# Performance work log

Measured on AMD Instinct MI355X. Metric: run time of the kernel, lower is better.

The kernel has to match this reference:

```python
import jax, jax.numpy as jnp
import numpy as np

TAU = 2.0        # LIF membrane time constant
VTH = 1.0        # spike threshold
VRESET = 0.0     # hard reset voltage
ALPHA = 2.0      # ATan surrogate alpha
LN_EPS = 1e-5


@jax.custom_vjp
def atan_spike(x):
    # Heaviside forward, ATan surrogate backward (spikingjelly surrogate.ATan)
    return (x >= 0.0).astype(x.dtype)

def _atan_fwd(x):
    return atan_spike(x), x

def _atan_bwd(x, g):
    z = (jnp.pi / 2.0) * ALPHA * x
    return (g * (ALPHA / 2.0) / (1.0 + z * z),)

atan_spike.defvjp(_atan_fwd, _atan_bwd)


def layer_norm(x, w, b):
    mu = jnp.mean(x, axis=-1, keepdims=True)
    var = jnp.mean(jnp.square(x - mu), axis=-1, keepdims=True)
    return (x - mu) * jax.lax.rsqrt(var + LN_EPS) * w + b


def time_shift(x):
    # x: [B,T,C] -> x shifted by one step in time, zero-padded at t=0
    return jnp.pad(x, ((0, 0), (1, 0), (0, 0)))[:, :-1]


def wkv(time_decay, time_first, k, v):
    # Numerically-stable RWKV WKV recurrence. k, v: [B,T,C]
    w = -jnp.exp(time_decay)  # [C]
    u = time_first            # [C]
    B, T, C = k.shape
    kT = jnp.moveaxis(k, 1, 0)  # [T,B,C]
    vT = jnp.moveaxis(v, 1, 0)
    init = (jnp.zeros((B, C), k.dtype),
            jnp.zeros((B, C), k.dtype),
            jnp.full((B, C), -1e38, k.dtype))

    def step(carry, kv_t):
        aa, bb, pp = carry
        kt, vt = kv_t
        ww = u + kt
        p = jnp.maximum(pp, ww)
        e1 = jnp.exp(pp - p)
        e2 = jnp.exp(ww - p)
        y = (e1 * aa + e2 * vt) / (e1 * bb + e2)
        ww2 = pp + w
        p2 = jnp.maximum(ww2, kt)
        e1b = jnp.exp(ww2 - p2)
        e2b = jnp.exp(kt - p2)
        return (e1b * aa + e2b * vt, e1b * bb + e2b, p2), y

    _, yT = jax.lax.scan(step, init, (kT, vT))
    return jnp.moveaxis(yT, 0, 1)  # [B,T,C]


def lif(x):
    # MultiStepLIFNode: tau=2, decay_input=True, v_th=1, hard reset to 0.
    # Recurrence runs over the sequence dim (permute(1,0,2) in torch is layout only).
    xT = jnp.moveaxis(x, 1, 0)  # [T,B,C]
    v0 = jnp.zeros_like(xT[0])

    def step(v, xt):
        v = v + (xt - (v - VRESET)) / TAU
        s = atan_spike(v - VTH)
        v = (1.0 - s) * v + s * VRESET
        return v, s

    _, sT = jax.lax.scan(step, v0, xT)
    return jnp.moveaxis(sT, 0, 1)


def rwkv_time_mix(x, time_decay, time_first, mix_k, mix_v, mix_r, Wk, Wv, Wr, Wo):
    xx = time_shift(x)
    xk = x * mix_k + xx * (1.0 - mix_k)
    xv = x * mix_v + xx * (1.0 - mix_v)
    xr = x * mix_r + xx * (1.0 - mix_r)
    k = jnp.einsum('btc,cd->btd', xk, Wk)
    v = jnp.einsum('btc,cd->btd', xv, Wv)
    r = jax.nn.sigmoid(jnp.einsum('btc,cd->btd', xr, Wr))
    y = wkv(time_decay, time_first, k, v)
    return jnp.einsum('btc,cd->btd', r * y, Wo)


def rwkv_channel_mix(x, mix_k, mix_r, Wk, Wv, Wr):
    xx = time_shift(x)
    xk = x * mix_k + xx * (1.0 - mix_k)
    xr = x * mix_r + xx * (1.0 - mix_r)
    k = jnp.square(jax.nn.relu(jnp.einsum('btc,ch->bth', xk, Wk)))  # relu^2
    kv = jnp.einsum('bth,hc->btc', k, Wv)
    return jax.nn.sigmoid(jnp.einsum('btc,cd->btd', xr, Wr)) * kv


def setup_inputs() -> dict:
    key = jax.random.key(0)
    B, T, C, H = 8, 2048, 768, 3072
    ks = jax.random.split(key, 20)
    p = lambda k, shape, s=0.02: (jax.random.normal(k, shape, jnp.float32) * s)
    u = lambda k, shape: jax.random.uniform(k, shape, jnp.float32)
    return {
        'x': jax.random.normal(ks[0], (B, T, C), jnp.float32),
        'ln1_w': jnp.ones((C,), jnp.float32), 'ln1_b': jnp.zeros((C,), jnp.float32),
        'ln2_w': jnp.ones((C,), jnp.float32), 'ln2_b': jnp.zeros((C,), jnp.float32),
        'att_time_decay': p(ks[1], (C,), 1.0),
        'att_time_first': p(ks[2], (C,), 1.0),
        'att_mix_k': u(ks[3], (C,)), 'att_mix_v': u(ks[4], (C,)), 'att_mix_r': u(ks[5], (C,)),
        'att_Wk': p(ks[6], (C, C)), 'att_Wv': p(ks[7], (C, C)),
        'att_Wr': p(ks[8], (C, C)), 'att_Wo': p(ks[9], (C, C)),
        'ffn_mix_k': u(ks[10], (C,)), 'ffn_mix_r': u(ks[11], (C,)),
        'ffn_Wk': p(ks[12], (C, H)), 'ffn_Wv': p(ks[13], (H, C)), 'ffn_Wr': p(ks[14], (C, C)),
    }


def reference(x, ln1_w, ln1_b, ln2_w, ln2_b,
              att_time_decay, att_time_first, att_mix_k, att_mix_v, att_mix_r,
              att_Wk, att_Wv, att_Wr, att_Wo,
              ffn_mix_k, ffn_mix_r, ffn_Wk, ffn_Wv, ffn_Wr):
    # Block.forward with layer_id != 0 (no ln0, att path); dropout in eval mode.
    a = rwkv_time_mix(layer_norm(x, ln1_w, ln1_b), att_time_decay, att_time_first,
                      att_mix_k, att_mix_v, att_mix_r, att_Wk, att_Wv, att_Wr, att_Wo)
    x = x + lif(a)
    f = rwkv_channel_mix(layer_norm(x, ln2_w, ln2_b), ffn_mix_k, ffn_mix_r,
                         ffn_Wk, ffn_Wv, ffn_Wr)
    x = x + lif(f)
    return x
```

## Files before the change

kernel.cpp:

```cpp
#include <hip/hip_runtime.h>

#define B_ 8
#define T_ 2048
#define C_ 768
#define H_ 3072
#define BT_ (B_ * T_)
#define BC_ (B_ * C_)
#define WSEG 64
#define NWSEG 32
#define LSEG 64
#define NLSEG 32
#define LWARM 96

typedef unsigned short u16;
typedef short bf16x8 __attribute__((ext_vector_type(8)));
typedef float f32x4 __attribute__((ext_vector_type(4)));

__device__ __forceinline__ float b2f(u16 u) {
    union { unsigned i; float f; } w; w.i = ((unsigned)u) << 16; return w.f;
}
__device__ __forceinline__ u16 f2b(float f) {
    union { float f; unsigned i; } w; w.f = f;
    return (u16)((w.i + 0x7fffu + ((w.i >> 16) & 1u)) >> 16);
}

typedef __attribute__((address_space(3))) unsigned int lds_u32;
typedef const __attribute__((address_space(1))) unsigned int glb_u32;
__device__ __forceinline__ void gld_lds16(const void* g, void* l) {
    __builtin_amdgcn_global_load_lds((glb_u32*)g, (lds_u32*)l, 16, 0, 0);
}

template<int NOUT>
__global__ __launch_bounds__(512)
void lnmixw(const float* __restrict__ x, const float* __restrict__ w,
            const float* __restrict__ b,
            const float* __restrict__ m1, const float* __restrict__ m2,
            const float* __restrict__ m3,
            u16* __restrict__ o1, u16* __restrict__ o2, u16* __restrict__ o3) {
    const int wv = threadIdx.x >> 6, lane = threadIdx.x & 63;
    const int row = blockIdx.x * 8 + wv;
    const int t = row % T_;
    const float4* xr4 = (const float4*)(x + (size_t)row * C_);
    const float4* xp4 = (const float4*)(x + (size_t)(row - 1) * C_);
    float4 c[3], p[3];
#pragma unroll
    for (int j = 0; j < 3; ++j) c[j] = xr4[lane + j * 64];
    if (t > 0) {
#pragma unroll
        for (int j = 0; j < 3; ++j) p[j] = xp4[lane + j * 64];
    } else {
#pragma unroll
        for (int j = 0; j < 3; ++j) p[j] = make_float4(0.f, 0.f, 0.f, 0.f);
    }
    float s = 0.f, s2 = 0.f, ps = 0.f, ps2 = 0.f;
#pragma unroll
    for (int j = 0; j < 3; ++j) {
        s += c[j].x + c[j].y + c[j].z + c[j].w;
        s2 += c[j].x * c[j].x + c[j].y * c[j].y + c[j].z * c[j].z + c[j].w * c[j].w;
        ps += p[j].x + p[j].y + p[j].z + p[j].w;
        ps2 += p[j].x * p[j].x + p[j].y * p[j].y + p[j].z * p[j].z + p[j].w * p[j].w;
    }
#pragma unroll
    for (int off = 32; off > 0; off >>= 1) {
        s += __shfl_down(s, off);  s2 += __shfl_down(s2, off);
        ps += __shfl_down(ps, off); ps2 += __shfl_down(ps2, off);
    }
    s = __shfl(s, 0); s2 = __shfl(s2, 0); ps = __shfl(ps, 0); ps2 = __shfl(ps2, 0);
    const float mu = s * (1.f / C_);
    const float rs = rsqrtf(s2 * (1.f / C_) - mu * mu + 1e-5f);
    const float pmu = ps * (1.f / C_);
    const float prs = rsqrtf(ps2 * (1.f / C_) - pmu * pmu + 1e-5f);
    const size_t ob = (size_t)row * C_;
#pragma unroll
    for (int j = 0; j < 3; ++j) {
        int fi = lane + j * 64;
        float4 w4 = ((const float4*)w)[fi];
        float4 b4 = ((const float4*)b)[fi];
        float4 n, np;
        n.x = (c[j].x - mu) * rs * w4.x + b4.x;
        n.y = (c[j].y - mu) * rs * w4.y + b4.y;
        n.z = (c[j].z - mu) * rs * w4.z + b4.z;
        n.w = (c[j].w - mu) * rs * w4.w + b4.w;
        if (t > 0) {
            np.x = (p[j].x - pmu) * prs * w4.x + b4.x;
            np.y = (p[j].y - pmu) * prs * w4.y + b4.y;
            np.z = (p[j].z - pmu) * prs * w4.z + b4.z;
            np.w = (p[j].w - pmu) * prs * w4.w + b4.w;
        } else {
            np = make_float4(0.f, 0.f, 0.f, 0.f);
        }
        float4 mm = ((const float4*)m1)[fi];
        ushort4 ov;
        ov.x = f2b(fmaf(mm.x, n.x - np.x, np.x));
        ov.y = f2b(fmaf(mm.y, n.y - np.y, np.y));
        ov.z = f2b(fmaf(mm.z, n.z - np.z, np.z));
        ov.w = f2b(fmaf(mm.w, n.w - np.w, np.w));
        *(ushort4*)(o1 + ob + fi * 4) = ov;
        mm = ((const float4*)m2)[fi];
        ov.x = f2b(fmaf(mm.x, n.x - np.x, np.x));
        ov.y = f2b(fmaf(mm.y, n.y - np.y, np.y));
        ov.z = f2b(fmaf(mm.z, n.z - np.z, np.z));
        ov.w = f2b(fmaf(mm.w, n.w - np.w, np.w));
        *(ushort4*)(o2 + ob + fi * 4) = ov;
        if constexpr (NOUT == 3) {
            mm = ((const float4*)m3)[fi];
            ov.x = f2b(fmaf(mm.x, n.x - np.x, np.x));
            ov.y = f2b(fmaf(mm.y, n.y - np.y, np.y));
            ov.z = f2b(fmaf(mm.z, n.z - np.z, np.z));
            ov.w = f2b(fmaf(mm.w, n.w - np.w, np.w));
            *(ushort4*)(o3 + ob + fi * 4) = ov;
        }
    }
}

struct TCJ { const float* s; u16* d; int R, Ncol, nbx, b0; };
struct TC7 { TCJ j[7]; };
__global__ void tcast_all(TC7 jobs) {
    __shared__ float t[32][33];
    int bid = blockIdx.x;
    int ji = 0;
#pragma unroll
    for (int k = 1; k < 7; ++k) if (bid >= jobs.j[k].b0) ji = k;
    TCJ jb = jobs.j[ji];
    int local = bid - jb.b0;
    int bx = local % jb.nbx, by = local / jb.nbx;
    int c0 = bx * 32, r0 = by * 32;
    int col = threadIdx.x & 31, rw = threadIdx.x >> 5;
#pragma unroll
    for (int i = 0; i < 4; ++i) {
        int r = rw + i * 8;
        t[r][col] = jb.s[(size_t)(r0 + r) * jb.Ncol + c0 + col];
    }
    __syncthreads();
#pragma unroll
    for (int i = 0; i < 4; ++i) {
        int r = rw + i * 8;
        jb.d[(size_t)(c0 + r) * jb.R + r0 + col] = f2b(t[col][r]);
    }
}

__device__ __forceinline__ void gemm_core128(const u16* __restrict__ A,
                                             const u16* __restrict__ WT,
                                             int K, int m0, int n0,
                                             u16* L, f32x4 acc[4][4]) {
    const int tid = threadIdx.x;
    const int lane = tid & 63, wid = tid >> 6;
    const int wr = wid >> 1, wc = wid & 1;
    const int r16 = lane & 15, g = lane >> 4;

    const int srow = tid >> 3;
    const int sunit = tid & 7;
    const int ssw = sunit ^ (srow & 7);
    const u16* gA = A + (size_t)(m0 + srow) * K + ssw * 8;
    const u16* gB = WT + (size_t)(n0 + srow) * K + ssw * 8;
    u16* lA = L + tid * 8;
    u16* lB = L + 8192 + tid * 8;

#define STGA(buf) do { \
        gld_lds16(gA,                  lA + (buf) * 16384); \
        gld_lds16(gA + (size_t)32 * K, lA + (buf) * 16384 + 2048); \
        gld_lds16(gA + (size_t)64 * K, lA + (buf) * 16384 + 4096); \
        gld_lds16(gA + (size_t)96 * K, lA + (buf) * 16384 + 6144); \
        gA += 64; } while (0)
#define STGB(buf) do { \
        gld_lds16(gB,                  lB + (buf) * 16384); \
        gld_lds16(gB + (size_t)32 * K, lB + (buf) * 16384 + 2048); \
        gld_lds16(gB + (size_t)64 * K, lB + (buf) * 16384 + 4096); \
        gld_lds16(gB + (size_t)96 * K, lB + (buf) * 16384 + 6144); \
        gB += 64; } while (0)

    int offA[4], offB[4];
#pragma unroll
    for (int m = 0; m < 4; ++m) {
        int row = wr * 64 + m * 16 + r16;
        offA[m] = row * 64 + (g ^ (row & 7)) * 8;
    }
#pragma unroll
    for (int n = 0; n < 4; ++n) {
        int rob = wc * 64 + n * 16 + r16;
        offB[n] = 8192 + rob * 64 + (g ^ (rob & 7)) * 8;
    }

    const int nt = K >> 6;
    STGA(0); STGB(0);
    asm volatile("s_waitcnt vmcnt(0)" ::: "memory");
    __builtin_amdgcn_sched_barrier(0);
    __builtin_amdgcn_s_barrier();

    for (int t = 0; t < nt; ++t) {
        const u16* Lb = L + (t & 1) * 16384;
        const bool stg = (t + 1 < nt);
        bf16x8 a0[4], b0[4];
#pragma unroll
        for (int m = 0; m < 4; ++m) a0[m] = *(const bf16x8*)(Lb + offA[m]);
#pragma unroll
        for (int n = 0; n < 4; ++n) b0[n] = *(const bf16x8*)(Lb + offB[n]);
        __builtin_amdgcn_sched_barrier(0);
        if (stg) { STGA((t + 1) & 1); STGB((t + 1) & 1); }
        asm volatile("s_waitcnt lgkmcnt(0)" ::: "memory");
        __builtin_amdgcn_sched_barrier(0);
        __builtin_amdgcn_s_setprio(1);
#pragma unroll
        for (int m = 0; m < 4; ++m)
#pragma unroll
            for (int n = 0; n < 4; ++n)
                acc[m][n] = __builtin_amdgcn_mfma_f32_16x16x32_bf16(a0[m], b0[n], acc[m][n], 0, 0, 0);
        __builtin_amdgcn_s_setprio(0);
        __builtin_amdgcn_sched_barrier(0);
        bf16x8 a1[4], b1[4];
#pragma unroll
        for (int m = 0; m < 4; ++m) a1[m] = *(const bf16x8*)(Lb + (offA[m] ^ 32));
#pragma unroll
        for (int n = 0; n < 4; ++n) b1[n] = *(const bf16x8*)(Lb + (offB[n] ^ 32));
        asm volatile("s_waitcnt lgkmcnt(0)" ::: "memory");
        __builtin_amdgcn_sched_barrier(0);
        __builtin_amdgcn_s_setprio(1);
#pragma unroll
        for (int m = 0; m < 4; ++m)
#pragma unroll
            for (int n = 0; n < 4; ++n)
                acc[m][n] = __builtin_amdgcn_mfma_f32_16x16x32_bf16(a1[m], b1[n], acc[m][n], 0, 0, 0);
        __builtin_amdgcn_s_setprio(0);
        __builtin_amdgcn_sched_barrier(0);
        if (stg) {
            asm volatile("s_waitcnt vmcnt(0)" ::: "memory");
            __builtin_amdgcn_sched_barrier(0);
            __builtin_amdgcn_s_barrier();
        }
    }
#undef STGA
#undef STGB
}

__device__ __forceinline__ void xcd_remap2(int& bx, int& by) {
    const int gx = gridDim.x;
    const int nwg = gx * gridDim.y;
    const int lin = blockIdx.y * gx + blockIdx.x;
    const int q = nwg >> 3, r = nwg & 7;
    const int xcd = lin & 7, pos = lin >> 3;
    const int nid = (xcd < r ? xcd * (q + 1) : r * (q + 1) + (xcd - r) * q) + pos;
    const int g4 = gx << 2;
    const int grp = nid / g4, rem = nid - grp * g4;
    by = (grp << 2) + (rem & 3);
    bx = rem >> 2;
}

__device__ __forceinline__ void epilogue128(f32x4 acc[4][4], u16* O, const u16* Emul,
                                            int m0, int n0, int N, int mode, bool emul) {
    const int lane = threadIdx.x & 63, wid = threadIdx.x >> 6;
    const int wr = wid >> 1, wc = wid & 1;
    const int r16 = lane & 15, g = lane >> 4;
#pragma unroll
    for (int m = 0; m < 4; ++m)
#pragma unroll
        for (int n = 0; n < 4; ++n)
#pragma unroll
            for (int j = 0; j < 4; ++j) {
                int row = m0 + wr * 64 + m * 16 + g * 4 + j;
                int col = n0 + wc * 64 + n * 16 + r16;
                float v = acc[m][n][j];
                if (mode == 1) v = 1.f / (1.f + expf(-v));
                else if (mode == 2) { v = fmaxf(v, 0.f); v = v * v; }
                size_t o = (size_t)row * N + col;
                if (emul) v *= b2f(Emul[o]);
                O[o] = f2b(v);
            }
}

template<int MODE, bool EMUL>
__global__ __launch_bounds__(256, 2)
void gemm128(const u16* __restrict__ A, const u16* __restrict__ WT,
             u16* __restrict__ Cout, const u16* __restrict__ Emul, int N, int K) {
    __shared__ u16 L[32768];
    int bx, by;
    xcd_remap2(bx, by);
    const int m0 = by << 7, n0 = bx << 7;
    f32x4 acc[4][4];
#pragma unroll
    for (int i = 0; i < 4; ++i)
#pragma unroll
        for (int j = 0; j < 4; ++j)
#pragma unroll
            for (int q = 0; q < 4; ++q) acc[i][j][q] = 0.f;
    gemm_core128(A, WT, K, m0, n0, L, acc);
    epilogue128(acc, Cout, Emul, m0, n0, N, MODE, EMUL);
}

struct P3 {
    const u16 *A0, *A1, *A2;
    const u16 *W0, *W1, *W2;
    u16 *O0, *O1, *O2;
};
__global__ __launch_bounds__(256, 2)
void proj3(P3 p, int N, int K) {
    __shared__ u16 L[32768];
    const int z = blockIdx.z;
    const u16* A = (z == 0) ? p.A0 : (z == 1) ? p.A1 : p.A2;
    const u16* W = (z == 0) ? p.W0 : (z == 1) ? p.W1 : p.W2;
    u16* O = (z == 0) ? p.O0 : (z == 1) ? p.O1 : p.O2;
    int bx, by;
    xcd_remap2(bx, by);
    const int m0 = by << 7, n0 = bx << 7;
    f32x4 acc[4][4];
#pragma unroll
    for (int i = 0; i < 4; ++i)
#pragma unroll
        for (int j = 0; j < 4; ++j)
#pragma unroll
            for (int q = 0; q < 4; ++q) acc[i][j][q] = 0.f;
    gemm_core128(A, W, K, m0, n0, L, acc);
    epilogue128(acc, O, nullptr, m0, n0, N, (z == 2) ? 1 : 0, false);
}

struct J2 {
    const u16 *A0, *W0; u16 *O0;
    const u16 *A1, *W1; u16 *O1;
};
__global__ __launch_bounds__(256, 2)
void ffn1rr(J2 p, int K) {
    __shared__ u16 L[32768];
    int bx, by;
    xcd_remap2(bx, by);
    const bool isF = (bx < 24);
    const u16* A = isF ? p.A0 : p.A1;
    const u16* W = isF ? p.W0 : p.W1;
    u16* O = isF ? p.O0 : p.O1;
    const int N = isF ? 3072 : 768;
    const int m0 = by << 7;
    const int n0 = (isF ? bx : bx - 24) << 7;
    f32x4 acc[4][4];
#pragma unroll
    for (int i = 0; i < 4; ++i)
#pragma unroll
        for (int j = 0; j < 4; ++j)
#pragma unroll
            for (int q = 0; q < 4; ++q) acc[i][j][q] = 0.f;
    gemm_core128(A, W, K, m0, n0, L, acc);
    epilogue128(acc, O, nullptr, m0, n0, N, isF ? 2 : 1, false);
}

__global__ void wkv_p1(const float* __restrict__ td, const u16* __restrict__ K,
                       const u16* __restrict__ V, float* __restrict__ st) {
    int idx = blockIdx.x * 256 + threadIdx.x;
    int seg = blockIdx.y;
    int c2 = idx * 2;
    int b = c2 / C_, c = c2 - b * C_;
    float w0 = -expf(td[c]), w1 = -expf(td[c + 1]);
    size_t off = (size_t)b * T_ * C_ + (size_t)seg * WSEG * C_ + c;
    float aa0 = 0.f, bb0 = 0.f, pp0 = -1e38f;
    float aa1 = 0.f, bb1 = 0.f, pp1 = -1e38f;
#pragma unroll 4
    for (int i = 0; i < WSEG; ++i) {
        ushort2 k2 = *(const ushort2*)(K + off + (size_t)i * C_);
        ushort2 v2 = *(const ushort2*)(V + off + (size_t)i * C_);
        {
            float kt = b2f(k2.x), vt = b2f(v2.x);
            float ww = pp0 + w0;
            float p = fmaxf(ww, kt);
            float e1 = expf(ww - p), e2 = expf(kt - p);
            aa0 = e1 * aa0 + e2 * vt; bb0 = e1 * bb0 + e2; pp0 = p;
        }
        {
            float kt = b2f(k2.y), vt = b2f(v2.y);
            float ww = pp1 + w1;
            float p = fmaxf(ww, kt);
            float e1 = expf(ww - p), e2 = expf(kt - p);
            aa1 = e1 * aa1 + e2 * vt; bb1 = e1 * bb1 + e2; pp1 = p;
        }
    }
    int sidx = seg * 3 * BC_ + b * C_ + c;
    *(float2*)(st + sidx) = make_float2(aa0, aa1);
    *(float2*)(st + sidx + BC_) = make_float2(bb0, bb1);
    *(float2*)(st + sidx + 2 * BC_) = make_float2(pp0, pp1);
}

__global__ void wkv_p3(const float* __restrict__ td, const float* __restrict__ tf,
                       const u16* __restrict__ K, const u16* __restrict__ V,
                       const u16* __restrict__ R, const float* __restrict__ st,
                       u16* __restrict__ RY) {
    int idx = blockIdx.x * 256 + threadIdx.x;
    int seg = blockIdx.y;
    int c2 = idx * 2;
    int b = c2 / C_, c = c2 - b * C_;
    float w0 = -expf(td[c]), w1 = -expf(td[c + 1]);
    float u0 = tf[c], u1 = tf[c + 1];
    float wL0 = w0 * (float)WSEG, wL1 = w1 * (float)WSEG;
    float aa0 = 0.f, bb0 = 0.f, pp0 = -1e38f;
    float aa1 = 0.f, bb1 = 0.f, pp1 = -1e38f;
    for (int s = 0; s < seg; ++s) {
        int sidx = s * 3 * BC_ + b * C_ + c;
        float2 la = *(const float2*)(st + sidx);
        float2 lb = *(const float2*)(st + sidx + BC_);
        float2 lp = *(const float2*)(st + sidx + 2 * BC_);
        {
            float ppw = pp0 + wL0;
            float p = fmaxf(ppw, lp.x);
            float e1 = expf(ppw - p), e2 = expf(lp.x - p);
            aa0 = e1 * aa0 + e2 * la.x; bb0 = e1 * bb0 + e2 * lb.x; pp0 = p;
        }
        {
            float ppw = pp1 + wL1;
            float p = fmaxf(ppw, lp.y);
            float e1 = expf(ppw - p), e2 = expf(lp.y - p);
            aa1 = e1 * aa1 + e2 * la.y; bb1 = e1 * bb1 + e2 * lb.y; pp1 = p;
        }
    }
    size_t off = (size_t)b * T_ * C_ + (size_t)seg * WSEG * C_ + c;
#pragma unroll 4
    for (int i = 0; i < WSEG; ++i) {
        ushort2 k2 = *(const ushort2*)(K + off + (size_t)i * C_);
        ushort2 v2 = *(const ushort2*)(V + off + (size_t)i * C_);
        ushort2 r2 = *(const ushort2*)(R + off + (size_t)i * C_);
        ushort2 o2v;
        {
            float kt = b2f(k2.x), vt = b2f(v2.x), rr = b2f(r2.x);
            float ww = u0 + kt;
            float p = fmaxf(pp0, ww);
            float e1 = expf(pp0 - p), e2 = expf(ww - p);
            o2v.x = f2b(rr * (e1 * aa0 + e2 * vt) / (e1 * bb0 + e2));
            float ww2 = pp0 + w0;
            float p2 = fmaxf(ww2, kt);
            float e1b = expf(ww2 - p2), e2b = expf(kt - p2);
            aa0 = e1b * aa0 + e2b * vt; bb0 = e1b * bb0 + e2b; pp0 = p2;
        }
        {
            float kt = b2f(k2.y), vt = b2f(v2.y), rr = b2f(r2.y);
            float ww = u1 + kt;
            float p = fmaxf(pp1, ww);
            float e1 = expf(pp1 - p), e2 = expf(ww - p);
            o2v.y = f2b(rr * (e1 * aa1 + e2 * vt) / (e1 * bb1 + e2));
            float ww2 = pp1 + w1;
            float p2 = fmaxf(ww2, kt);
            float e1b = expf(ww2 - p2), e2b = expf(kt - p2);
            aa1 = e1b * aa1 + e2b * vt; bb1 = e1b * bb1 + e2b; pp1 = p2;
        }
        *(ushort2*)(RY + off + (size_t)i * C_) = o2v;
    }
}

__global__ void lif_add_b(const u16* __restrict__ cur, const float* __restrict__ base,
                          float* __restrict__ out) {
    int idx = blockIdx.x * 256 + threadIdx.x;
    int seg = blockIdx.y;
    int c2 = idx * 2;
    int b = c2 / C_, c = c2 - b * C_;
    size_t rowbase = (size_t)b * T_ * C_ + c;
    int t0 = seg * LSEG;
    int tw = t0 - LWARM; if (tw < 0) tw = 0;
    int nw = t0 - tw;
    float v0 = 0.f, v1 = 0.f;
    const u16* cp = cur + rowbase + (size_t)tw * C_;
#pragma unroll 8
    for (int i = 0; i < nw; ++i) {
        ushort2 x2 = *(const ushort2*)(cp + (size_t)i * C_);
        v0 += (b2f(x2.x) - v0) * 0.5f;
        v0 = (v0 >= 1.f) ? 0.f : v0;
        v1 += (b2f(x2.y) - v1) * 0.5f;
        v1 = (v1 >= 1.f) ? 0.f : v1;
    }
    const u16* cq = cur + rowbase + (size_t)t0 * C_;
    const float* bp = base + rowbase + (size_t)t0 * C_;
    float* op = out + rowbase + (size_t)t0 * C_;
#pragma unroll 8
    for (int i = 0; i < LSEG; ++i) {
        ushort2 x2 = *(const ushort2*)(cq + (size_t)i * C_);
        float2 b2 = *(const float2*)(bp + (size_t)i * C_);
        v0 += (b2f(x2.x) - v0) * 0.5f;
        float s0 = (v0 >= 1.f) ? 1.f : 0.f;
        v1 += (b2f(x2.y) - v1) * 0.5f;
        float s1 = (v1 >= 1.f) ? 1.f : 0.f;
        *(float2*)(op + (size_t)i * C_) = make_float2(b2.x + s0, b2.y + s1);
        v0 = (s0 > 0.f) ? 0.f : v0;
        v1 = (s1 > 0.f) ? 0.f : v1;
    }
}

extern "C" void kernel_launch(void* const* d_in, const int* in_sizes, int n_in,
                              void* d_out, int out_size, void* d_ws, size_t ws_size,
                              hipStream_t stream) {
    const float* x    = (const float*)d_in[0];
    const float* ln1w = (const float*)d_in[1];
    const float* ln1b = (const float*)d_in[2];
    const float* ln2w = (const float*)d_in[3];
    const float* ln2b = (const float*)d_in[4];
    const float* td   = (const float*)d_in[5];
    const float* tf   = (const float*)d_in[6];
    const float* amk  = (const float*)d_in[7];
    const float* amv  = (const float*)d_in[8];
    const float* amr  = (const float*)d_in[9];
    const float* aWk  = (const float*)d_in[10];
    const float* aWv  = (const float*)d_in[11];
    const float* aWr  = (const float*)d_in[12];
    const float* aWo  = (const float*)d_in[13];
    const float* fmk  = (const float*)d_in[14];
    const float* fmr  = (const float*)d_in[15];
    const float* fWk  = (const float*)d_in[16];
    const float* fWv  = (const float*)d_in[17];
    const float* fWr  = (const float*)d_in[18];
    float* out = (float*)d_out;

    const size_t NBC = (size_t)BT_ * C_;
    u16* WkT = (u16*)d_ws;
    u16* WvT = WkT + 589824;
    u16* WrT = WvT + 589824;
    u16* WoT = WrT + 589824;
    u16* FrT = WoT + 589824;
    u16* FkT = FrT + 589824;
    u16* FvT = FkT + 2359296;
    float* st  = (float*)(FvT + 2359296);
    u16* S0 = (u16*)(st + NWSEG * 3 * BC_);
    u16* S1 = S0 + NBC;
    u16* S2 = S1 + NBC;
    u16* S3 = S2 + NBC;
    u16* Hbuf = S3 + NBC;
    size_t fixed_b = (size_t)((char*)Hbuf - (char*)d_ws);

    int NCH = 4;
    if (ws_size >= fixed_b + ((size_t)BT_ * H_ + NBC) * 2) NCH = 1;
    else if (ws_size >= fixed_b + ((size_t)(BT_ / 2) * H_ + NBC / 2) * 2) NCH = 2;
    const int CH = BT_ / NCH;
    u16* Fbuf = Hbuf + (size_t)CH * H_;

    u16* Kb = (u16*)d_out;
    u16* Vb = Kb + NBC;

    {
        TC7 jobs;
        const float* srcs[7] = {aWk, aWv, aWr, aWo, fWr, fWk, fWv};
        u16* dsts[7] = {WkT, WvT, WrT, WoT, FrT, FkT, FvT};
        int Rs[7]    = {768, 768, 768, 768, 768, 768, 3072};
        int Ns[7]    = {768, 768, 768, 768, 768, 3072, 768};
        int b0 = 0;
        for (int k = 0; k < 7; ++k) {
            jobs.j[k].s = srcs[k]; jobs.j[k].d = dsts[k];
            jobs.j[k].R = Rs[k]; jobs.j[k].Ncol = Ns[k];
            jobs.j[k].nbx = Ns[k] / 32; jobs.j[k].b0 = b0;
            b0 += (Ns[k] / 32) * (Rs[k] / 32);
        }
        tcast_all<<<b0, 256, 0, stream>>>(jobs);
    }

    lnmixw<3><<<BT_ / 8, 512, 0, stream>>>(x, ln1w, ln1b, amk, amv, amr, S0, S1, S2);
    {
        P3 p{S0, S1, S2, WkT, WvT, WrT, Kb, Vb, S3};
        proj3<<<dim3(6, 128, 3), 256, 0, stream>>>(p, C_, C_);
    }
    wkv_p1<<<dim3(BC_ / 512, NWSEG), 256, 0, stream>>>(td, Kb, Vb, st);
    wkv_p3<<<dim3(BC_ / 512, NWSEG), 256, 0, stream>>>(td, tf, Kb, Vb, S3, st, S0);
    gemm128<0, false><<<dim3(6, 128), 256, 0, stream>>>(S0, WoT, S1, nullptr, C_, C_);
    lif_add_b<<<dim3(BC_ / 512, NLSEG), 256, 0, stream>>>(S1, x, out);
    lnmixw<2><<<BT_ / 8, 512, 0, stream>>>(out, ln2w, ln2b, fmk, fmr, nullptr, S0, S1, nullptr);

    if (NCH == 1) {
        J2 p{S0, FkT, Hbuf, S1, FrT, S2};
        ffn1rr<<<dim3(30, 128), 256, 0, stream>>>(p, C_);
        gemm128<0, true><<<dim3(6, 128), 256, 0, stream>>>(Hbuf, FvT, Fbuf, S2, C_, H_);
        lif_add_b<<<dim3(BC_ / 512, NLSEG), 256, 0, stream>>>(Fbuf, out, out);
    } else {
        gemm128<1, false><<<dim3(6, 128), 256, 0, stream>>>(S1, FrT, S2, nullptr, C_, C_);
        for (int ch = 0; ch < NCH; ++ch) {
            const u16* xk2c = S0 + (size_t)ch * CH * C_;
            const u16* rrc  = S2 + (size_t)ch * CH * C_;
            gemm128<2, false><<<dim3(24, CH / 128), 256, 0, stream>>>(xk2c, FkT, Hbuf, nullptr, H_, C_);
            gemm128<0, true><<<dim3(6, CH / 128), 256, 0, stream>>>(Hbuf, FvT, Fbuf, rrc, C_, H_);
            lif_add_b<<<dim3((CH / T_) * C_ / 512, NLSEG), 256, 0, stream>>>(
                Fbuf, out + (size_t)ch * CH * C_, out + (size_t)ch * CH * C_);
        }
    }
}
```

Measured before the change: 522.9 us.

## Halve GEMM K-tile to 32 and raise occupancy to four blocks per CU

The shared GEMM core now stages K-tiles of 32 instead of 64, which halves the LDS footprint to 32KB per block and changes the swizzle to suit the narrower rows. Launch bounds go from 2 to 4 blocks per CU, so more waves can hide memory latency. In exchange there are twice as many iterations and barriers per K, less MFMA work between syncs, and a tighter register budget at 4 blocks that may cause spills.

After: 525.0 us. Within noise of the previous version (+0.4%).

```diff
diff --git a/kernel.cpp b/kernel.cpp
--- a/kernel.cpp
+++ b/kernel.cpp
@@ -148,53 +148,49 @@
     const int wr = wid >> 1, wc = wid & 1;
     const int r16 = lane & 15, g = lane >> 4;
 
-    const int srow = tid >> 3;
-    const int sunit = tid & 7;
-    const int ssw = sunit ^ (srow & 7);
+    const int srow = tid >> 2;
+    const int sunit = tid & 3;
+    const int ssw = sunit ^ ((srow >> 1) & 3);
     const u16* gA = A + (size_t)(m0 + srow) * K + ssw * 8;
     const u16* gB = WT + (size_t)(n0 + srow) * K + ssw * 8;
     u16* lA = L + tid * 8;
-    u16* lB = L + 8192 + tid * 8;
+    u16* lB = L + 4096 + tid * 8;
 
 #define STGA(buf) do { \
-        gld_lds16(gA,                  lA + (buf) * 16384); \
-        gld_lds16(gA + (size_t)32 * K, lA + (buf) * 16384 + 2048); \
-        gld_lds16(gA + (size_t)64 * K, lA + (buf) * 16384 + 4096); \
-        gld_lds16(gA + (size_t)96 * K, lA + (buf) * 16384 + 6144); \
-        gA += 64; } while (0)
+        gld_lds16(gA,                  lA + (buf) * 8192); \
+        gld_lds16(gA + (size_t)64 * K, lA + (buf) * 8192 + 2048); \
+        gA += 32; } while (0)
 #define STGB(buf) do { \
-        gld_lds16(gB,                  lB + (buf) * 16384); \
-        gld_lds16(gB + (size_t)32 * K, lB + (buf) * 16384 + 2048); \
-        gld_lds16(gB + (size_t)64 * K, lB + (buf) * 16384 + 4096); \
-        gld_lds16(gB + (size_t)96 * K, lB + (buf) * 16384 + 6144); \
-        gB += 64; } while (0)
+        gld_lds16(gB,                  lB + (buf) * 8192); \
+        gld_lds16(gB + (size_t)64 * K, lB + (buf) * 8192 + 2048); \
+        gB += 32; } while (0)
 
     int offA[4], offB[4];
 #pragma unroll
     for (int m = 0; m < 4; ++m) {
         int row = wr * 64 + m * 16 + r16;
-        offA[m] = row * 64 + (g ^ (row & 7)) * 8;
+        offA[m] = row * 32 + (g ^ ((row >> 1) & 3)) * 8;
     }
 #pragma unroll
     for (int n = 0; n < 4; ++n) {
         int rob = wc * 64 + n * 16 + r16;
-        offB[n] = 8192 + rob * 64 + (g ^ (rob & 7)) * 8;
-    }
-
-    const int nt = K >> 6;
+        offB[n] = 4096 + rob * 32 + (g ^ ((rob >> 1) & 3)) * 8;
+    }
+
+    const int nt = K >> 5;
     STGA(0); STGB(0);
     asm volatile("s_waitcnt vmcnt(0)" ::: "memory");
     __builtin_amdgcn_sched_barrier(0);
     __builtin_amdgcn_s_barrier();
 
     for (int t = 0; t < nt; ++t) {
-        const u16* Lb = L + (t & 1) * 16384;
+        const u16* Lb = L + (t & 1) * 8192;
         const bool stg = (t + 1 < nt);
-        bf16x8 a0[4], b0[4];
-#pragma unroll
-        for (int m = 0; m < 4; ++m) a0[m] = *(const bf16x8*)(Lb + offA[m]);
-#pragma unroll
-        for (int n = 0; n < 4; ++n) b0[n] = *(const bf16x8*)(Lb + offB[n]);
+        bf16x8 af[4], bg[4];
+#pragma unroll
+        for (int m = 0; m < 4; ++m) af[m] = *(const bf16x8*)(Lb + offA[m]);
+#pragma unroll
+        for (int n = 0; n < 4; ++n) bg[n] = *(const bf16x8*)(Lb + offB[n]);
         __builtin_amdgcn_sched_barrier(0);
         if (stg) { STGA((t + 1) & 1); STGB((t + 1) & 1); }
         asm volatile("s_waitcnt lgkmcnt(0)" ::: "memory");
@@ -204,22 +200,7 @@
         for (int m = 0; m < 4; ++m)
 #pragma unroll
             for (int n = 0; n < 4; ++n)
-                acc[m][n] = __builtin_amdgcn_mfma_f32_16x16x32_bf16(a0[m], b0[n], acc[m][n], 0, 0, 0);
-        __builtin_amdgcn_s_setprio(0);
-        __builtin_amdgcn_sched_barrier(0);
-        bf16x8 a1[4], b1[4];
-#pragma unroll
-        for (int m = 0; m < 4; ++m) a1[m] = *(const bf16x8*)(Lb + (offA[m] ^ 32));
-#pragma unroll
-        for (int n = 0; n < 4; ++n) b1[n] = *(const bf16x8*)(Lb + (offB[n] ^ 32));
-        asm volatile("s_waitcnt lgkmcnt(0)" ::: "memory");
-        __builtin_amdgcn_sched_barrier(0);
-        __builtin_amdgcn_s_setprio(1);
-#pragma unroll
-        for (int m = 0; m < 4; ++m)
-#pragma unroll
-            for (int n = 0; n < 4; ++n)
-                acc[m][n] = __builtin_amdgcn_mfma_f32_16x16x32_bf16(a1[m], b1[n], acc[m][n], 0, 0, 0);
+                acc[m][n] = __builtin_amdgcn_mfma_f32_16x16x32_bf16(af[m], bg[n], acc[m][n], 0, 0, 0);
         __builtin_amdgcn_s_setprio(0);
         __builtin_amdgcn_sched_barrier(0);
         if (stg) {
@@ -268,10 +249,10 @@
 }
 
 template<int MODE, bool EMUL>
-__global__ __launch_bounds__(256, 2)
+__global__ __launch_bounds__(256, 4)
 void gemm128(const u16* __restrict__ A, const u16* __restrict__ WT,
              u16* __restrict__ Cout, const u16* __restrict__ Emul, int N, int K) {
-    __shared__ u16 L[32768];
+    __shared__ u16 L[16384];
     int bx, by;
     xcd_remap2(bx, by);
     const int m0 = by << 7, n0 = bx << 7;
@@ -291,9 +272,9 @@
     const u16 *W0, *W1, *W2;
     u16 *O0, *O1, *O2;
 };
-__global__ __launch_bounds__(256, 2)
+__global__ __launch_bounds__(256, 4)
 void proj3(P3 p, int N, int K) {
-    __shared__ u16 L[32768];
+    __shared__ u16 L[16384];
     const int z = blockIdx.z;
     const u16* A = (z == 0) ? p.A0 : (z == 1) ? p.A1 : p.A2;
     const u16* W = (z == 0) ? p.W0 : (z == 1) ? p.W1 : p.W2;
@@ -316,9 +297,9 @@
     const u16 *A0, *W0; u16 *O0;
     const u16 *A1, *W1; u16 *O1;
 };
-__global__ __launch_bounds__(256, 2)
+__global__ __launch_bounds__(256, 4)
 void ffn1rr(J2 p, int K) {
-    __shared__ u16 L[32768];
+    __shared__ u16 L[16384];
     int bx, by;
     xcd_remap2(bx, by);
     const bool isF = (bx < 24);
```
